# Kernel optimization log

Measured on AMD Instinct MI355X. Metric: run time of the kernel, lower is better.

## Reference

```python
import jax, jax.numpy as jnp
import numpy as np
from jax import lax

DN = ('NCHW', 'HWIO', 'NCHW')

def conv(x, w, b, stride, pad):
    y = lax.conv_general_dilated(x, w, (stride, stride), ((pad, pad), (pad, pad)),
                                 dimension_numbers=DN)
    return y + b[None, :, None, None]

def deconv(x, w, b):
    # PyTorch ConvTranspose2d(k=4, s=2, p=1) == conv with lhs_dilation=2, padding=k-1-p=2
    y = lax.conv_general_dilated(x, w, (1, 1), ((2, 2), (2, 2)), lhs_dilation=(2, 2),
                                 dimension_numbers=DN)
    return y + b[None, :, None, None]

def setup_inputs() -> dict:
    key = jax.random.key(0)
    ks = jax.random.split(key, 16)
    B, K, D = 4096, 512, 64
    def w(k, shape, fan_in):
        s = 1.0 / np.sqrt(fan_in)
        return jax.random.uniform(k, shape, jnp.float32, -s, s)
    return {
        'x': jax.random.uniform(ks[0], (B, 1, 28, 28), jnp.float32),
        # encoder
        'w1': w(ks[1], (4, 4, 1, 32), 4 * 4 * 1),  'b1': w(ks[2], (32,), 4 * 4 * 1),
        'w2': w(ks[3], (4, 4, 32, 64), 4 * 4 * 32), 'b2': w(ks[4], (64,), 4 * 4 * 32),
        'w3': w(ks[5], (1, 1, 64, D), 64),          'b3': w(ks[6], (D,), 64),
        # codebook, init uniform(-1/K, 1/K) as in the torch module
        'codebook': jax.random.uniform(ks[7], (K, D), jnp.float32, -1.0 / K, 1.0 / K),
        # decoder
        'dw0': w(ks[8], (1, 1, D, 64), D),          'db0': w(ks[9], (64,), D),
        'dw1': w(ks[10], (4, 4, 64, 32), 4 * 4 * 64), 'db1': w(ks[11], (32,), 4 * 4 * 64),
        'dw2': w(ks[12], (4, 4, 32, 1), 4 * 4 * 32),  'db2': w(ks[13], (1,), 4 * 4 * 32),
    }

def vector_quantize(z_perm, codebook, commitment_cost=0.25):
    # z_perm: [B, H, W, D]
    D = codebook.shape[1]
    flat_z = z_perm.reshape(-1, D)                                      # [N, D]
    dists = (jnp.sum(flat_z * flat_z, axis=1, keepdims=True)
             + jnp.sum(codebook * codebook, axis=1)
             - 2.0 * flat_z @ codebook.T)                               # [N, K]
    indices = jnp.argmin(dists, axis=1)                                 # [N]
    quantized = codebook[indices].reshape(z_perm.shape)                 # [B, H, W, D]
    e_latent = jnp.mean((quantized - lax.stop_gradient(z_perm)) ** 2)
    q_latent = jnp.mean((z_perm - lax.stop_gradient(quantized)) ** 2)
    vq_loss = e_latent + commitment_cost * q_latent
    quantized_st = z_perm + lax.stop_gradient(quantized - z_perm)
    return quantized_st, vq_loss, indices.reshape(z_perm.shape[:-1])

def reference(x, w1, b1, w2, b2, w3, b3, codebook, dw0, db0, dw1, db1, dw2, db2):
    # encoder: 28 -> 14 -> 7
    h = jax.nn.relu(conv(x, w1, b1, 2, 1))
    h = jax.nn.relu(conv(h, w2, b2, 2, 1))
    z = conv(h, w3, b3, 1, 0)                        # [B, D, 7, 7]
    z_perm = jnp.transpose(z, (0, 2, 3, 1))          # [B, 7, 7, D]
    zq_perm, vq_loss, indices = vector_quantize(z_perm, codebook)
    z_q = jnp.transpose(zq_perm, (0, 3, 1, 2))       # [B, D, 7, 7]
    # decoder: 7 -> 14 -> 28
    d = conv(z_q, dw0, db0, 1, 0)
    d = jax.nn.relu(deconv(d, dw1, db1))
    recon = jax.nn.sigmoid(deconv(d, dw2, db2))
    recon = recon[:, :, :28, :28]
    return recon, z, z_q, vq_loss, indices
```

## Files before the change

kernel.cpp:

```cpp
#include <hip/hip_runtime.h>


#define NB 4096

__device__ __forceinline__ float4 f4fma(float s, float4 w, float4 a) {
  a.x = fmaf(s, w.x, a.x); a.y = fmaf(s, w.y, a.y);
  a.z = fmaf(s, w.z, a.z); a.w = fmaf(s, w.w, a.w);
  return a;
}
__device__ __forceinline__ float4 f4relu(float4 a) {
  a.x = fmaxf(a.x, 0.f); a.y = fmaxf(a.y, 0.f);
  a.z = fmaxf(a.z, 0.f); a.w = fmaxf(a.w, 0.f);
  return a;
}
__device__ __forceinline__ float4 f4addrn(float4 a, float4 b) {
  a.x = __fadd_rn(a.x, b.x); a.y = __fadd_rn(a.y, b.y);
  a.z = __fadd_rn(a.z, b.z); a.w = __fadd_rn(a.w, b.w);
  return a;
}

__device__ __forceinline__ float np_sumsq64(const float* v) {
  float r[8];
#pragma unroll
  for (int j = 0; j < 8; ++j) r[j] = __fmul_rn(v[j], v[j]);
#pragma unroll
  for (int i = 8; i < 64; i += 8)
#pragma unroll
    for (int j = 0; j < 8; ++j) r[j] = __fadd_rn(r[j], __fmul_rn(v[i + j], v[i + j]));
  return __fadd_rn(__fadd_rn(__fadd_rn(r[0], r[1]), __fadd_rn(r[2], r[3])),
                   __fadd_rn(__fadd_rn(r[4], r[5]), __fadd_rn(r[6], r[7])));
}

__global__ __launch_bounds__(256) void k0_init(const float* __restrict__ cb,
                                               float* __restrict__ cn,
                                               float* __restrict__ loss) {
  int t = threadIdx.x;
  if (t == 0) *loss = 0.f;
  for (int k = t; k < 512; k += 256) cn[k] = np_sumsq64(&cb[k * 64]);
}

__global__ __launch_bounds__(256) void k1_conv1(const float* __restrict__ x,
                                                const float* __restrict__ w1,
                                                const float* __restrict__ b1,
                                                float* __restrict__ h1) {
  __shared__ float xs[784];
  __shared__ float wl[512];
  __shared__ float bs[32];
  int n = blockIdx.x, t = threadIdx.x;
  for (int j = t; j < 784; j += 256) xs[j] = x[n * 784 + j];
  for (int j = t; j < 512; j += 256) wl[j] = w1[j];
  if (t < 32) bs[t] = b1[t];
  __syncthreads();
  int c = t & 31, pg = t >> 5;
  for (int s = pg; s < 196; s += 8) {
    int oh = s / 14, ow = s % 14;
    float acc = 0.f;
#pragma unroll
    for (int kh = 0; kh < 4; ++kh) {
      int ih = 2 * oh - 1 + kh;
      if (ih < 0 || ih >= 28) continue;
#pragma unroll
      for (int kw = 0; kw < 4; ++kw) {
        int iw = 2 * ow - 1 + kw;
        if (iw < 0 || iw >= 28) continue;
        acc = fmaf(xs[ih * 28 + iw], wl[(kh * 4 + kw) * 32 + c], acc);
      }
    }
    acc = __fadd_rn(acc, bs[c]);
    h1[(n * 196 + s) * 32 + c] = fmaxf(acc, 0.f);
  }
}

__global__ __launch_bounds__(256) void k2_conv2(const float* __restrict__ h1,
                                                const float* __restrict__ w2,
                                                const float* __restrict__ b2,
                                                float* __restrict__ h2) {
  __shared__ float4 xs4[2 * 2049];
  int nb = blockIdx.x, t = threadIdx.x;
  size_t n0 = (size_t)nb * 2;
  for (int j = t; j < 4098; j += 256) xs4[j] = make_float4(0.f, 0.f, 0.f, 0.f);
  __syncthreads();
  for (int j = t; j < 1568; j += 256) {
    int p = j >> 3, c4 = j & 7;
    int ihp = p / 14 + 1, iwp = p % 14 + 1;
    int chunk = (c4 * 16 + ihp) * 16 + (iwp & 1) * 8 + (iwp >> 1);
    xs4[chunk] = *(const float4*)(h1 + n0 * 6272 + p * 32 + c4 * 4);
    xs4[2049 + chunk] = *(const float4*)(h1 + (n0 + 1) * 6272 + p * 32 + c4 * 4);
  }
  __syncthreads();
  int l = t & 63;
  int co0 = __builtin_amdgcn_readfirstlane((t >> 6) * 16);
  int img = l >> 5, pt = l & 31;
  int oh0 = pt >> 3, ow = pt & 7;
  int imgoff = img * 2049;
  bool v0 = (ow < 7);
  bool v1 = (ow < 7) && (oh0 + 4 < 7);
  float4 A0[4], A1[4];
#pragma unroll
  for (int g = 0; g < 4; ++g) { A0[g] = make_float4(0.f, 0.f, 0.f, 0.f); A1[g] = A0[g]; }
#pragma unroll 1
  for (int kk = 0; kk < 16; ++kk) {
    int kh = kk >> 2, kw = kk & 3;
    int cc = 2 * ow + kw; if (cc > 15) cc = 15;
    int off = (cc & 1) * 8 + (cc >> 1);
    int rc0 = 2 * oh0 + kh;
    int rc1 = rc0 + 8; if (rc1 > 15) rc1 = 15;
    int b0 = imgoff + rc0 * 16 + off;
    int b1 = imgoff + rc1 * 16 + off;
    int wb = __builtin_amdgcn_readfirstlane(kk * 2048 + co0);
#pragma unroll 2
    for (int c4 = 0; c4 < 8; ++c4) {
      float4 x0 = xs4[b0 + c4 * 256];
      float4 x1 = xs4[b1 + c4 * 256];
      float xa0[4] = {x0.x, x0.y, x0.z, x0.w};
      float xa1[4] = {x1.x, x1.y, x1.z, x1.w};
      const float* wk = w2 + wb + c4 * 256;
#pragma unroll
      for (int j = 0; j < 4; ++j) {
#pragma unroll
        for (int g = 0; g < 4; ++g) {
          float4 wv4;
          wv4.x = wk[j * 64 + g * 4 + 0]; wv4.y = wk[j * 64 + g * 4 + 1];
          wv4.z = wk[j * 64 + g * 4 + 2]; wv4.w = wk[j * 64 + g * 4 + 3];
          A0[g] = f4fma(xa0[j], wv4, A0[g]);
          A1[g] = f4fma(xa1[j], wv4, A1[g]);
        }
      }
    }
  }
  float4 bias[4];
#pragma unroll
  for (int g = 0; g < 4; ++g) bias[g] = *(const float4*)&b2[co0 + g * 4];
  if (v0) {
    size_t ob = ((n0 + img) * 49 + oh0 * 7 + ow) * 64 + co0;
#pragma unroll
    for (int g = 0; g < 4; ++g)
      *(float4*)&h2[ob + g * 4] = f4relu(f4addrn(A0[g], bias[g]));
  }
  if (v1) {
    size_t ob = ((n0 + img) * 49 + (oh0 + 4) * 7 + ow) * 64 + co0;
#pragma unroll
    for (int g = 0; g < 4; ++g)
      *(float4*)&h2[ob + g * 4] = f4relu(f4addrn(A1[g], bias[g]));
  }
}

__global__ __launch_bounds__(256) void k_pw(const float* __restrict__ xin,
                                            const float* __restrict__ w,
                                            const float* __restrict__ bias,
                                            float* __restrict__ yout) {
  __shared__ float tile[256 * 65];
  int t = threadIdx.x;
  long m0 = (long)blockIdx.x * 256;
  for (int j = t; j < 16384; j += 256) tile[(j >> 6) * 65 + (j & 63)] = xin[m0 * 64 + j];
  __syncthreads();
  float xr[64];
#pragma unroll
  for (int ci = 0; ci < 64; ++ci) xr[ci] = tile[t * 65 + ci];
  for (int g = 0; g < 4; ++g) {
    float4 z4 = make_float4(0.f, 0.f, 0.f, 0.f);
    float4 a0 = z4, a1 = z4, a2 = z4, a3 = z4;
#pragma unroll
    for (int ci = 0; ci < 64; ++ci) {
      float xv = xr[ci];
      const float* wr = &w[ci * 64 + g * 16];
      a0 = f4fma(xv, *(const float4*)&wr[0], a0);
      a1 = f4fma(xv, *(const float4*)&wr[4], a1);
      a2 = f4fma(xv, *(const float4*)&wr[8], a2);
      a3 = f4fma(xv, *(const float4*)&wr[12], a3);
    }
    a0 = f4addrn(a0, *(const float4*)&bias[g * 16 + 0]);
    a1 = f4addrn(a1, *(const float4*)&bias[g * 16 + 4]);
    a2 = f4addrn(a2, *(const float4*)&bias[g * 16 + 8]);
    a3 = f4addrn(a3, *(const float4*)&bias[g * 16 + 12]);
    float* dst = &tile[t * 65 + g * 16];
    dst[0] = a0.x; dst[1] = a0.y; dst[2] = a0.z; dst[3] = a0.w;
    dst[4] = a1.x; dst[5] = a1.y; dst[6] = a1.z; dst[7] = a1.w;
    dst[8] = a2.x; dst[9] = a2.y; dst[10] = a2.z; dst[11] = a2.w;
    dst[12] = a3.x; dst[13] = a3.y; dst[14] = a3.z; dst[15] = a3.w;
  }
  __syncthreads();
  for (int j = t; j < 16384; j += 256) yout[m0 * 64 + j] = tile[(j >> 6) * 65 + (j & 63)];
}

__global__ __launch_bounds__(256) void k4_vq(const float* __restrict__ zin,
                                             const float* __restrict__ cb,
                                             const float* __restrict__ cn,
                                             float* __restrict__ zq_nhwc,
                                             float* __restrict__ outz,
                                             float* __restrict__ outzq,
                                             float* __restrict__ outidx,
                                             float* __restrict__ loss) {
  __shared__ float tile[256 * 65];
  __shared__ float red[4];
  int t = threadIdx.x;
  long m0 = (long)blockIdx.x * 256;
  for (int j = t; j < 16384; j += 256) tile[(j >> 6) * 65 + (j & 63)] = zin[m0 * 64 + j];
  __syncthreads();
  float zr[64];
#pragma unroll
  for (int ci = 0; ci < 64; ++ci) zr[ci] = tile[t * 65 + ci];
  unsigned m = (unsigned)(m0 + t);
  unsigned n = m / 49u, sp = m % 49u;
  float* zob = outz + (size_t)n * 3136 + sp;
#pragma unroll
  for (int ci = 0; ci < 64; ++ci) zob[ci * 49] = zr[ci];
  float sz = np_sumsq64(zr);
  float minv = 3.4e38f; int mini = 0;
  for (int k = 0; k < 512; ++k) {
    float d = 0.f;
#pragma unroll
    for (int ci = 0; ci < 64; ci += 4) {
      float4 c4 = *(const float4*)&cb[k * 64 + ci];
      d = fmaf(zr[ci + 0], c4.x, d);
      d = fmaf(zr[ci + 1], c4.y, d);
      d = fmaf(zr[ci + 2], c4.z, d);
      d = fmaf(zr[ci + 3], c4.w, d);
    }
    float dist = __fsub_rn(__fadd_rn(sz, cn[k]), __fmul_rn(2.f, d));
    if (dist < minv) { minv = dist; mini = k; }
  }
  outidx[m] = (float)mini;
  float* qob = outzq + (size_t)n * 3136 + sp;
  float lsum = 0.f;
#pragma unroll
  for (int ci = 0; ci < 64; ci += 4) {
    float4 q4 = *(const float4*)&cb[mini * 64 + ci];
    float* dst = &tile[t * 65 + ci];
    dst[0] = q4.x; dst[1] = q4.y; dst[2] = q4.z; dst[3] = q4.w;
    qob[(ci + 0) * 49] = q4.x; qob[(ci + 1) * 49] = q4.y;
    qob[(ci + 2) * 49] = q4.z; qob[(ci + 3) * 49] = q4.w;
    float e0 = q4.x - zr[ci + 0], e1 = q4.y - zr[ci + 1];
    float e2 = q4.z - zr[ci + 2], e3 = q4.w - zr[ci + 3];
    lsum = fmaf(e0, e0, lsum); lsum = fmaf(e1, e1, lsum);
    lsum = fmaf(e2, e2, lsum); lsum = fmaf(e3, e3, lsum);
  }
#pragma unroll
  for (int off = 32; off > 0; off >>= 1) lsum += __shfl_down(lsum, off);
  int wid = t >> 6, lane = t & 63;
  if (lane == 0) red[wid] = lsum;
  __syncthreads();
  if (t == 0) atomicAdd(loss, red[0] + red[1] + red[2] + red[3]);
  for (int j = t; j < 16384; j += 256) zq_nhwc[m0 * 64 + j] = tile[(j >> 6) * 65 + (j & 63)];
}

__global__ __launch_bounds__(64) void k_lossfin(const float* __restrict__ loss,
                                                float* __restrict__ out) {
  if (threadIdx.x == 0) out[0] = loss[0] * (1.25f / 12845056.f);
}

__global__ __launch_bounds__(256) void k6_deconv1(const float* __restrict__ d0,
                                                  const float* __restrict__ dw1,
                                                  const float* __restrict__ db1,
                                                  float* __restrict__ d1) {
  __shared__ float4 xs4[2 * 1297];
  int nb = blockIdx.x, t = threadIdx.x;
  size_t n0 = (size_t)nb * 2;
  for (int j = t; j < 2594; j += 256) xs4[j] = make_float4(0.f, 0.f, 0.f, 0.f);
  __syncthreads();
  for (int j = t; j < 784; j += 256) {
    int p = j >> 4, c4 = j & 15;
    int chunk = c4 * 81 + (p / 7 + 1) * 9 + (p % 7 + 1);
    xs4[chunk] = *(const float4*)(d0 + n0 * 3136 + p * 64 + c4 * 4);
    xs4[1297 + chunk] = *(const float4*)(d0 + (n0 + 1) * 3136 + p * 64 + c4 * 4);
  }
  __syncthreads();
  int l = t & 63;
  int ph = __builtin_amdgcn_readfirstlane(t >> 6);
  int ra = ph >> 1, rb = ph & 1;
  int img = l >> 5, pt = l & 31;
  bool v1 = (pt + 32 < 49);
  int p1 = v1 ? pt + 32 : 48;
  int mh0 = pt / 7, mw0 = pt % 7;
  int mh1 = p1 / 7, mw1 = p1 % 7;
  int imgoff = img * 1297;
  float4 A0[8], A1[8];
#pragma unroll
  for (int g = 0; g < 8; ++g) { A0[g] = make_float4(0.f, 0.f, 0.f, 0.f); A1[g] = A0[g]; }
#pragma unroll 1
  for (int tap = 0; tap < 4; ++tap) {
    int th = tap >> 1, tw = tap & 1;
    int kh = 2 * th + ra, kw = 2 * tw + rb;
    int b0 = imgoff + (mh0 + th + ra) * 9 + (mw0 + tw + rb);
    int b1 = imgoff + (mh1 + th + ra) * 9 + (mw1 + tw + rb);
    int wb = __builtin_amdgcn_readfirstlane((kh * 4 + kw) * 2048);
#pragma unroll 1
    for (int c4 = 0; c4 < 16; ++c4) {
      float4 x0 = xs4[b0 + c4 * 81];
      float4 x1 = xs4[b1 + c4 * 81];
      float xa0[4] = {x0.x, x0.y, x0.z, x0.w};
      float xa1[4] = {x1.x, x1.y, x1.z, x1.w};
      const float* wk = dw1 + wb + c4 * 128;
#pragma unroll
      for (int j = 0; j < 4; ++j) {
#pragma unroll
        for (int g = 0; g < 8; ++g) {
          float4 wv4;
          wv4.x = wk[j * 32 + g * 4 + 0]; wv4.y = wk[j * 32 + g * 4 + 1];
          wv4.z = wk[j * 32 + g * 4 + 2]; wv4.w = wk[j * 32 + g * 4 + 3];
          A0[g] = f4fma(xa0[j], wv4, A0[g]);
          A1[g] = f4fma(xa1[j], wv4, A1[g]);
        }
      }
    }
  }
  int oh0 = 2 * mh0 + ra, ow0 = 2 * mw0 + rb;
  size_t ob0 = ((n0 + img) * 196 + (size_t)(oh0 * 14 + ow0)) * 32;
#pragma unroll
  for (int g = 0; g < 8; ++g) {
    float4 bg = *(const float4*)&db1[g * 4];
    *(float4*)&d1[ob0 + g * 4] = f4relu(f4addrn(A0[g], bg));
  }
  if (v1) {
    int oh1 = 2 * mh1 + ra, ow1 = 2 * mw1 + rb;
    size_t ob1 = ((n0 + img) * 196 + (size_t)(oh1 * 14 + ow1)) * 32;
#pragma unroll
    for (int g = 0; g < 8; ++g) {
      float4 bg = *(const float4*)&db1[g * 4];
      *(float4*)&d1[ob1 + g * 4] = f4relu(f4addrn(A1[g], bg));
    }
  }
}

__global__ __launch_bounds__(256) void k7_deconv2(const float* __restrict__ d1,
                                                  const float* __restrict__ dw2,
                                                  const float* __restrict__ db2,
                                                  float* __restrict__ recon) {
  __shared__ float xs[196 * 36];
  __shared__ float wl[512];
  int n = blockIdx.x, t = threadIdx.x;
  for (int j = t; j < 6272; j += 256) xs[(j >> 5) * 36 + (j & 31)] = d1[(size_t)n * 6272 + j];
  for (int j = t; j < 512; j += 256) wl[j] = dw2[j];
  __syncthreads();
  float bias = db2[0];
  for (int j = t; j < 392; j += 256) {
    int ra = j / 196, rem = j % 196;
    int mh = rem / 14, mw = rem % 14;
    float acc0 = bias, acc1 = bias;
    bool vm = (mw >= 1), vp = (mw + 1 < 14);
#pragma unroll
    for (int th = 0; th < 2; ++th) {
      int ih = mh + th - 1 + ra;
      if (ih < 0 || ih >= 14) continue;
      int kh = 2 * th + ra;
#pragma unroll
      for (int ci = 0; ci < 32; ci += 4) {
        float4 z4 = make_float4(0.f, 0.f, 0.f, 0.f);
        float4 xm = vm ? *(float4*)&xs[(ih * 14 + mw - 1) * 36 + ci] : z4;
        float4 x0 = *(float4*)&xs[(ih * 14 + mw) * 36 + ci];
        float4 xp = vp ? *(float4*)&xs[(ih * 14 + mw + 1) * 36 + ci] : z4;
        float4 wk0 = *(float4*)&wl[(kh * 4 + 0) * 32 + ci];
        float4 wk1 = *(float4*)&wl[(kh * 4 + 1) * 32 + ci];
        float4 wk2 = *(float4*)&wl[(kh * 4 + 2) * 32 + ci];
        float4 wk3 = *(float4*)&wl[(kh * 4 + 3) * 32 + ci];
        acc0 = fmaf(xm.x, wk0.x, acc0); acc0 = fmaf(xm.y, wk0.y, acc0);
        acc0 = fmaf(xm.z, wk0.z, acc0); acc0 = fmaf(xm.w, wk0.w, acc0);
        acc0 = fmaf(x0.x, wk2.x, acc0); acc0 = fmaf(x0.y, wk2.y, acc0);
        acc0 = fmaf(x0.z, wk2.z, acc0); acc0 = fmaf(x0.w, wk2.w, acc0);
        acc1 = fmaf(x0.x, wk1.x, acc1); acc1 = fmaf(x0.y, wk1.y, acc1);
        acc1 = fmaf(x0.z, wk1.z, acc1); acc1 = fmaf(x0.w, wk1.w, acc1);
        acc1 = fmaf(xp.x, wk3.x, acc1); acc1 = fmaf(xp.y, wk3.y, acc1);
        acc1 = fmaf(xp.z, wk3.z, acc1); acc1 = fmaf(xp.w, wk3.w, acc1);
      }
    }
    float r0 = 1.f / (1.f + __expf(-acc0));
    float r1 = 1.f / (1.f + __expf(-acc1));
    int oh = 2 * mh + ra;
    *(float2*)&recon[(size_t)n * 784 + oh * 28 + 2 * mw] = make_float2(r0, r1);
  }
}

extern "C" void kernel_launch(void* const* d_in, const int* in_sizes, int n_in,
                              void* d_out, int out_size, void* d_ws, size_t ws_size,
                              hipStream_t stream) {
  const float* x   = (const float*)d_in[0];
  const float* w1  = (const float*)d_in[1];
  const float* b1  = (const float*)d_in[2];
  const float* w2  = (const float*)d_in[3];
  const float* b2  = (const float*)d_in[4];
  const float* w3  = (const float*)d_in[5];
  const float* b3  = (const float*)d_in[6];
  const float* cb  = (const float*)d_in[7];
  const float* dw0 = (const float*)d_in[8];
  const float* db0 = (const float*)d_in[9];
  const float* dw1 = (const float*)d_in[10];
  const float* db1 = (const float*)d_in[11];
  const float* dw2 = (const float*)d_in[12];
  const float* db2 = (const float*)d_in[13];
  float* out = (float*)d_out;
  float* ws  = (float*)d_ws;

  float* h1   = ws;
  float* h2   = ws + 25690112;
  float* zb   = ws + 38535168;
  float* cn   = ws + 51380224;
  float* loss = ws + 51380736;

  float* recon   = out;
  float* zout    = out + 3211264;
  float* zqout   = out + 16056320;
  float* lossout = out + 28901376;
  float* idxout  = out + 28901377;

  k0_init<<<1, 256, 0, stream>>>(cb, cn, loss);
  k1_conv1<<<NB, 256, 0, stream>>>(x, w1, b1, h1);
  k2_conv2<<<NB / 2, 256, 0, stream>>>(h1, w2, b2, h2);
  k_pw<<<784, 256, 0, stream>>>(h2, w3, b3, zb);
  k4_vq<<<784, 256, 0, stream>>>(zb, cb, cn, h2, zout, zqout, idxout, loss);
  k_lossfin<<<1, 64, 0, stream>>>(loss, lossout);
  k_pw<<<784, 256, 0, stream>>>(h2, dw0, db0, zb);
  k6_deconv1<<<NB / 2, 256, 0, stream>>>(zb, dw1, db1, h1);
  k7_deconv2<<<NB, 256, 0, stream>>>(h1, dw2, db2, recon);
}
```

Baseline: 1.255 ms.

## Fuse decoder 1x1 conv into VQ kernel and drop shared-memory transposes

Folds the decoder pointwise conv (dw0/db0) into the VQ kernel, so each thread applies it directly to its selected codebook row and writes the result in place into the z buffer. This removes one kernel launch and a full round trip of the quantized NHWC tensor. The pointwise and VQ kernels now read and write 64-float rows per thread with float4 accesses instead of staging through padded shared tiles. The VQ distance loop now handles four codewords per iteration, and the loss reduction uses a per-wave atomic with no block-level sync. In exchange, per-thread accesses are strided by 256 bytes rather than coalesced, and register pressure rises from the 64 accumulators.

```diff
diff --git a/kernel.cpp b/kernel.cpp
--- a/kernel.cpp
+++ b/kernel.cpp
@@ -149,99 +149,117 @@
                                             const float* __restrict__ w,
                                             const float* __restrict__ bias,
                                             float* __restrict__ yout) {
-  __shared__ float tile[256 * 65];
-  int t = threadIdx.x;
-  long m0 = (long)blockIdx.x * 256;
-  for (int j = t; j < 16384; j += 256) tile[(j >> 6) * 65 + (j & 63)] = xin[m0 * 64 + j];
-  __syncthreads();
+  size_t m = (size_t)blockIdx.x * 256 + threadIdx.x;
+  const float* xp = xin + m * 64;
   float xr[64];
 #pragma unroll
-  for (int ci = 0; ci < 64; ++ci) xr[ci] = tile[t * 65 + ci];
-  for (int g = 0; g < 4; ++g) {
-    float4 z4 = make_float4(0.f, 0.f, 0.f, 0.f);
-    float4 a0 = z4, a1 = z4, a2 = z4, a3 = z4;
-#pragma unroll
-    for (int ci = 0; ci < 64; ++ci) {
-      float xv = xr[ci];
-      const float* wr = &w[ci * 64 + g * 16];
-      a0 = f4fma(xv, *(const float4*)&wr[0], a0);
-      a1 = f4fma(xv, *(const float4*)&wr[4], a1);
-      a2 = f4fma(xv, *(const float4*)&wr[8], a2);
-      a3 = f4fma(xv, *(const float4*)&wr[12], a3);
-    }
-    a0 = f4addrn(a0, *(const float4*)&bias[g * 16 + 0]);
-    a1 = f4addrn(a1, *(const float4*)&bias[g * 16 + 4]);
-    a2 = f4addrn(a2, *(const float4*)&bias[g * 16 + 8]);
-    a3 = f4addrn(a3, *(const float4*)&bias[g * 16 + 12]);
-    float* dst = &tile[t * 65 + g * 16];
-    dst[0] = a0.x; dst[1] = a0.y; dst[2] = a0.z; dst[3] = a0.w;
-    dst[4] = a1.x; dst[5] = a1.y; dst[6] = a1.z; dst[7] = a1.w;
-    dst[8] = a2.x; dst[9] = a2.y; dst[10] = a2.z; dst[11] = a2.w;
-    dst[12] = a3.x; dst[13] = a3.y; dst[14] = a3.z; dst[15] = a3.w;
-  }
-  __syncthreads();
-  for (int j = t; j < 16384; j += 256) yout[m0 * 64 + j] = tile[(j >> 6) * 65 + (j & 63)];
-}
-
-__global__ __launch_bounds__(256) void k4_vq(const float* __restrict__ zin,
+  for (int c4 = 0; c4 < 16; ++c4) {
+    float4 v = *(const float4*)(xp + c4 * 4);
+    xr[c4 * 4 + 0] = v.x; xr[c4 * 4 + 1] = v.y;
+    xr[c4 * 4 + 2] = v.z; xr[c4 * 4 + 3] = v.w;
+  }
+  float4 A[16];
+#pragma unroll
+  for (int g = 0; g < 16; ++g) A[g] = make_float4(0.f, 0.f, 0.f, 0.f);
+#pragma unroll 1
+  for (int ci = 0; ci < 64; ++ci) {
+    float xv = xr[ci];
+    const float* wr = w + ci * 64;
+#pragma unroll
+    for (int g = 0; g < 16; ++g)
+      A[g] = f4fma(xv, *(const float4*)(wr + g * 4), A[g]);
+  }
+  float* yp = yout + m * 64;
+#pragma unroll
+  for (int g = 0; g < 16; ++g)
+    *(float4*)(yp + g * 4) = f4addrn(A[g], *(const float4*)(bias + g * 4));
+}
+
+__global__ __launch_bounds__(256) void k4_vq(float* __restrict__ zbuf,
                                              const float* __restrict__ cb,
                                              const float* __restrict__ cn,
-                                             float* __restrict__ zq_nhwc,
+                                             const float* __restrict__ dw0,
+                                             const float* __restrict__ db0,
                                              float* __restrict__ outz,
                                              float* __restrict__ outzq,
                                              float* __restrict__ outidx,
                                              float* __restrict__ loss) {
-  __shared__ float tile[256 * 65];
-  __shared__ float red[4];
   int t = threadIdx.x;
-  long m0 = (long)blockIdx.x * 256;
-  for (int j = t; j < 16384; j += 256) tile[(j >> 6) * 65 + (j & 63)] = zin[m0 * 64 + j];
-  __syncthreads();
+  size_t m = (size_t)blockIdx.x * 256 + t;
+  const float* zp = zbuf + m * 64;
   float zr[64];
 #pragma unroll
-  for (int ci = 0; ci < 64; ++ci) zr[ci] = tile[t * 65 + ci];
-  unsigned m = (unsigned)(m0 + t);
-  unsigned n = m / 49u, sp = m % 49u;
+  for (int c4 = 0; c4 < 16; ++c4) {
+    float4 v = *(const float4*)(zp + c4 * 4);
+    zr[c4 * 4 + 0] = v.x; zr[c4 * 4 + 1] = v.y;
+    zr[c4 * 4 + 2] = v.z; zr[c4 * 4 + 3] = v.w;
+  }
+  unsigned n = (unsigned)(m / 49u), sp = (unsigned)(m % 49u);
   float* zob = outz + (size_t)n * 3136 + sp;
 #pragma unroll
   for (int ci = 0; ci < 64; ++ci) zob[ci * 49] = zr[ci];
   float sz = np_sumsq64(zr);
   float minv = 3.4e38f; int mini = 0;
-  for (int k = 0; k < 512; ++k) {
-    float d = 0.f;
+#pragma unroll 1
+  for (int k = 0; k < 512; k += 4) {
+    const float* cp = cb + (size_t)k * 64;
+    float d0_ = 0.f, d1_ = 0.f, d2_ = 0.f, d3_ = 0.f;
 #pragma unroll
     for (int ci = 0; ci < 64; ci += 4) {
-      float4 c4 = *(const float4*)&cb[k * 64 + ci];
-      d = fmaf(zr[ci + 0], c4.x, d);
-      d = fmaf(zr[ci + 1], c4.y, d);
-      d = fmaf(zr[ci + 2], c4.z, d);
-      d = fmaf(zr[ci + 3], c4.w, d);
-    }
-    float dist = __fsub_rn(__fadd_rn(sz, cn[k]), __fmul_rn(2.f, d));
-    if (dist < minv) { minv = dist; mini = k; }
+      float4 a = *(const float4*)(cp + ci);
+      float4 b = *(const float4*)(cp + 64 + ci);
+      float4 c = *(const float4*)(cp + 128 + ci);
+      float4 e = *(const float4*)(cp + 192 + ci);
+      d0_ = fmaf(zr[ci], a.x, d0_); d0_ = fmaf(zr[ci + 1], a.y, d0_);
+      d0_ = fmaf(zr[ci + 2], a.z, d0_); d0_ = fmaf(zr[ci + 3], a.w, d0_);
+      d1_ = fmaf(zr[ci], b.x, d1_); d1_ = fmaf(zr[ci + 1], b.y, d1_);
+      d1_ = fmaf(zr[ci + 2], b.z, d1_); d1_ = fmaf(zr[ci + 3], b.w, d1_);
+      d2_ = fmaf(zr[ci], c.x, d2_); d2_ = fmaf(zr[ci + 1], c.y, d2_);
+      d2_ = fmaf(zr[ci + 2], c.z, d2_); d2_ = fmaf(zr[ci + 3], c.w, d2_);
+      d3_ = fmaf(zr[ci], e.x, d3_); d3_ = fmaf(zr[ci + 1], e.y, d3_);
+      d3_ = fmaf(zr[ci + 2], e.z, d3_); d3_ = fmaf(zr[ci + 3], e.w, d3_);
+    }
+    float q0 = __fsub_rn(__fadd_rn(sz, cn[k + 0]), __fmul_rn(2.f, d0_));
+    float q1 = __fsub_rn(__fadd_rn(sz, cn[k + 1]), __fmul_rn(2.f, d1_));
+    float q2 = __fsub_rn(__fadd_rn(sz, cn[k + 2]), __fmul_rn(2.f, d2_));
+    float q3 = __fsub_rn(__fadd_rn(sz, cn[k + 3]), __fmul_rn(2.f, d3_));
+    if (q0 < minv) { minv = q0; mini = k; }
+    if (q1 < minv) { minv = q1; mini = k + 1; }
+    if (q2 < minv) { minv = q2; mini = k + 2; }
+    if (q3 < minv) { minv = q3; mini = k + 3; }
   }
   outidx[m] = (float)mini;
   float* qob = outzq + (size_t)n * 3136 + sp;
+  const float* qrow = cb + (size_t)mini * 64;
   float lsum = 0.f;
-#pragma unroll
-  for (int ci = 0; ci < 64; ci += 4) {
-    float4 q4 = *(const float4*)&cb[mini * 64 + ci];
-    float* dst = &tile[t * 65 + ci];
-    dst[0] = q4.x; dst[1] = q4.y; dst[2] = q4.z; dst[3] = q4.w;
-    qob[(ci + 0) * 49] = q4.x; qob[(ci + 1) * 49] = q4.y;
-    qob[(ci + 2) * 49] = q4.z; qob[(ci + 3) * 49] = q4.w;
-    float e0 = q4.x - zr[ci + 0], e1 = q4.y - zr[ci + 1];
-    float e2 = q4.z - zr[ci + 2], e3 = q4.w - zr[ci + 3];
+  float4 A[16];
+#pragma unroll
+  for (int g = 0; g < 16; ++g) A[g] = make_float4(0.f, 0.f, 0.f, 0.f);
+#pragma unroll
+  for (int c4 = 0; c4 < 16; ++c4) {
+    float4 q4 = *(const float4*)(qrow + c4 * 4);
+    qob[(c4 * 4 + 0) * 49] = q4.x; qob[(c4 * 4 + 1) * 49] = q4.y;
+    qob[(c4 * 4 + 2) * 49] = q4.z; qob[(c4 * 4 + 3) * 49] = q4.w;
+    float e0 = q4.x - zr[c4 * 4 + 0], e1 = q4.y - zr[c4 * 4 + 1];
+    float e2 = q4.z - zr[c4 * 4 + 2], e3 = q4.w - zr[c4 * 4 + 3];
     lsum = fmaf(e0, e0, lsum); lsum = fmaf(e1, e1, lsum);
     lsum = fmaf(e2, e2, lsum); lsum = fmaf(e3, e3, lsum);
+    float qa[4] = {q4.x, q4.y, q4.z, q4.w};
+#pragma unroll
+    for (int j = 0; j < 4; ++j) {
+      const float* wr = dw0 + (c4 * 4 + j) * 64;
+#pragma unroll
+      for (int g = 0; g < 16; ++g)
+        A[g] = f4fma(qa[j], *(const float4*)(wr + g * 4), A[g]);
+    }
   }
 #pragma unroll
   for (int off = 32; off > 0; off >>= 1) lsum += __shfl_down(lsum, off);
-  int wid = t >> 6, lane = t & 63;
-  if (lane == 0) red[wid] = lsum;
-  __syncthreads();
-  if (t == 0) atomicAdd(loss, red[0] + red[1] + red[2] + red[3]);
-  for (int j = t; j < 16384; j += 256) zq_nhwc[m0 * 64 + j] = tile[(j >> 6) * 65 + (j & 63)];
+  if ((t & 63) == 0) atomicAdd(loss, lsum);
+  float* dst = zbuf + m * 64;
+#pragma unroll
+  for (int g = 0; g < 16; ++g)
+    *(float4*)(dst + g * 4) = f4addrn(A[g], *(const float4*)(db0 + g * 4));
 }
 
 __global__ __launch_bounds__(64) void k_lossfin(const float* __restrict__ loss,
@@ -406,9 +424,9 @@
   k1_conv1<<<NB, 256, 0, stream>>>(x, w1, b1, h1);
   k2_conv2<<<NB / 2, 256, 0, stream>>>(h1, w2, b2, h2);
   k_pw<<<784, 256, 0, stream>>>(h2, w3, b3, zb);
-  k4_vq<<<784, 256, 0, stream>>>(zb, cb, cn, h2, zout, zqout, idxout, loss);
+  k4_vq<<<784, 256, 0, stream>>>(zb, cb, cn, dw0, db0,
+                                 zout, zqout, idxout, loss);
   k_lossfin<<<1, 64, 0, stream>>>(loss, lossout);
-  k_pw<<<784, 256, 0, stream>>>(h2, dw0, db0, zb);
   k6_deconv1<<<NB / 2, 256, 0, stream>>>(zb, dw1, db1, h1);
   k7_deconv2<<<NB, 256, 0, stream>>>(h1, dw2, db2, recon);
 }
```

Result: slower. 2.316 ms (+84.6%).

## Stage codebook chunks in LDS and process two rows per thread in VQ

Applied to the files above, without the earlier changes.

The VQ kernel now handles 512 rows per block, with two latent vectors per thread, and loads the codebook into shared memory in 64-entry chunks instead of reading it from global memory in the inner loop. Each codebook float4 is then reused across two rows and two codes per iteration. The grid halves to 392 blocks and staging goes through a smaller LDS tile in four passes. This raises register pressure (128 floats of z per thread) and lowers block count, so occupancy and parallelism across the GPU drop.

```diff
diff --git a/kernel.cpp b/kernel.cpp
--- a/kernel.cpp
+++ b/kernel.cpp
@@ -191,57 +191,129 @@
                                              float* __restrict__ outzq,
                                              float* __restrict__ outidx,
                                              float* __restrict__ loss) {
-  __shared__ float tile[256 * 65];
+  __shared__ float lds[8320];
   __shared__ float red[4];
   int t = threadIdx.x;
-  long m0 = (long)blockIdx.x * 256;
-  for (int j = t; j < 16384; j += 256) tile[(j >> 6) * 65 + (j & 63)] = zin[m0 * 64 + j];
-  __syncthreads();
-  float zr[64];
-#pragma unroll
-  for (int ci = 0; ci < 64; ++ci) zr[ci] = tile[t * 65 + ci];
-  unsigned m = (unsigned)(m0 + t);
-  unsigned n = m / 49u, sp = m % 49u;
-  float* zob = outz + (size_t)n * 3136 + sp;
-#pragma unroll
-  for (int ci = 0; ci < 64; ++ci) zob[ci * 49] = zr[ci];
-  float sz = np_sumsq64(zr);
-  float minv = 3.4e38f; int mini = 0;
-  for (int k = 0; k < 512; ++k) {
-    float d = 0.f;
-#pragma unroll
-    for (int ci = 0; ci < 64; ci += 4) {
-      float4 c4 = *(const float4*)&cb[k * 64 + ci];
-      d = fmaf(zr[ci + 0], c4.x, d);
-      d = fmaf(zr[ci + 1], c4.y, d);
-      d = fmaf(zr[ci + 2], c4.z, d);
-      d = fmaf(zr[ci + 3], c4.w, d);
-    }
-    float dist = __fsub_rn(__fadd_rn(sz, cn[k]), __fmul_rn(2.f, d));
-    if (dist < minv) { minv = dist; mini = k; }
-  }
-  outidx[m] = (float)mini;
-  float* qob = outzq + (size_t)n * 3136 + sp;
+  size_t m0 = (size_t)blockIdx.x * 512;
+  float zrA[64], zrB[64];
+
+#define K4_STAGE_IN(S, ZR)                                                    \
+  {                                                                           \
+    __syncthreads();                                                          \
+    const float* src = zin + (m0 + (S) * 128) * 64;                           \
+    for (int j4 = t; j4 < 2048; j4 += 256) {                                  \
+      int row = j4 >> 4, col = (j4 & 15) * 4;                                 \
+      *(float4*)&lds[row * 65 + col] = *(const float4*)(src + j4 * 4);        \
+    }                                                                         \
+    __syncthreads();                                                          \
+    if ((t >> 7) == ((S) & 1)) {                                              \
+      int r = t & 127;                                                        \
+      _Pragma("unroll")                                                       \
+      for (int ci = 0; ci < 64; ci += 4) {                                    \
+        float4 v = *(float4*)&lds[r * 65 + ci];                               \
+        ZR[ci] = v.x; ZR[ci + 1] = v.y; ZR[ci + 2] = v.z; ZR[ci + 3] = v.w;   \
+      }                                                                       \
+    }                                                                         \
+  }
+
+  K4_STAGE_IN(0, zrA)
+  K4_STAGE_IN(1, zrA)
+  K4_STAGE_IN(2, zrB)
+  K4_STAGE_IN(3, zrB)
+
+  float szA = np_sumsq64(zrA), szB = np_sumsq64(zrB);
+  float minA = 3.4e38f, minB = 3.4e38f;
+  int miA = 0, miB = 0;
+#pragma unroll 1
+  for (int ch = 0; ch < 8; ++ch) {
+    __syncthreads();
+    for (int j = t; j < 4096; j += 256) lds[j] = cb[ch * 4096 + j];
+    if (ch == 0)
+      for (int j = t; j < 512; j += 256) lds[4096 + j] = cn[j];
+    __syncthreads();
+#pragma unroll 1
+    for (int k = 0; k < 64; k += 2) {
+      const float* r0 = &lds[k * 64];
+      const float* r1 = r0 + 64;
+      float dA0 = 0.f, dA1 = 0.f, dB0 = 0.f, dB1 = 0.f;
+#pragma unroll
+      for (int ci = 0; ci < 64; ci += 4) {
+        float4 c0 = *(const float4*)(r0 + ci);
+        float4 c1 = *(const float4*)(r1 + ci);
+        dA0 = fmaf(zrA[ci], c0.x, dA0); dA0 = fmaf(zrA[ci + 1], c0.y, dA0);
+        dA0 = fmaf(zrA[ci + 2], c0.z, dA0); dA0 = fmaf(zrA[ci + 3], c0.w, dA0);
+        dB0 = fmaf(zrB[ci], c0.x, dB0); dB0 = fmaf(zrB[ci + 1], c0.y, dB0);
+        dB0 = fmaf(zrB[ci + 2], c0.z, dB0); dB0 = fmaf(zrB[ci + 3], c0.w, dB0);
+        dA1 = fmaf(zrA[ci], c1.x, dA1); dA1 = fmaf(zrA[ci + 1], c1.y, dA1);
+        dA1 = fmaf(zrA[ci + 2], c1.z, dA1); dA1 = fmaf(zrA[ci + 3], c1.w, dA1);
+        dB1 = fmaf(zrB[ci], c1.x, dB1); dB1 = fmaf(zrB[ci + 1], c1.y, dB1);
+        dB1 = fmaf(zrB[ci + 2], c1.z, dB1); dB1 = fmaf(zrB[ci + 3], c1.w, dB1);
+      }
+      float cn0 = lds[4096 + ch * 64 + k];
+      float cn1 = lds[4096 + ch * 64 + k + 1];
+      float qA0 = __fsub_rn(__fadd_rn(szA, cn0), __fmul_rn(2.f, dA0));
+      float qA1 = __fsub_rn(__fadd_rn(szA, cn1), __fmul_rn(2.f, dA1));
+      float qB0 = __fsub_rn(__fadd_rn(szB, cn0), __fmul_rn(2.f, dB0));
+      float qB1 = __fsub_rn(__fadd_rn(szB, cn1), __fmul_rn(2.f, dB1));
+      int kk = ch * 64 + k;
+      if (qA0 < minA) { minA = qA0; miA = kk; }
+      if (qA1 < minA) { minA = qA1; miA = kk + 1; }
+      if (qB0 < minB) { minB = qB0; miB = kk; }
+      if (qB1 < minB) { minB = qB1; miB = kk + 1; }
+    }
+  }
+  outidx[m0 + t] = (float)miA;
+  outidx[m0 + 256 + t] = (float)miB;
+  {
+    unsigned mA = (unsigned)(m0 + t), mB = (unsigned)(m0 + 256 + t);
+    unsigned nA = mA / 49u, spA = mA % 49u;
+    unsigned nB = mB / 49u, spB = mB % 49u;
+    float* zoA = outz + (size_t)nA * 3136 + spA;
+    float* zoB = outz + (size_t)nB * 3136 + spB;
+#pragma unroll
+    for (int ci = 0; ci < 64; ++ci) { zoA[ci * 49] = zrA[ci]; zoB[ci * 49] = zrB[ci]; }
+  }
   float lsum = 0.f;
-#pragma unroll
-  for (int ci = 0; ci < 64; ci += 4) {
-    float4 q4 = *(const float4*)&cb[mini * 64 + ci];
-    float* dst = &tile[t * 65 + ci];
-    dst[0] = q4.x; dst[1] = q4.y; dst[2] = q4.z; dst[3] = q4.w;
-    qob[(ci + 0) * 49] = q4.x; qob[(ci + 1) * 49] = q4.y;
-    qob[(ci + 2) * 49] = q4.z; qob[(ci + 3) * 49] = q4.w;
-    float e0 = q4.x - zr[ci + 0], e1 = q4.y - zr[ci + 1];
-    float e2 = q4.z - zr[ci + 2], e3 = q4.w - zr[ci + 3];
-    lsum = fmaf(e0, e0, lsum); lsum = fmaf(e1, e1, lsum);
-    lsum = fmaf(e2, e2, lsum); lsum = fmaf(e3, e3, lsum);
-  }
+#define K4_STAGE_OUT(S, ZR, MI)                                               \
+  {                                                                           \
+    __syncthreads();                                                          \
+    if ((t >> 7) == ((S) & 1)) {                                              \
+      int r = t & 127;                                                        \
+      unsigned mm = (unsigned)(m0 + (S) * 128 + r);                           \
+      unsigned nn = mm / 49u, ss = mm % 49u;                                  \
+      float* qo = outzq + (size_t)nn * 3136 + ss;                             \
+      const float* qr = cb + (size_t)(MI) * 64;                               \
+      _Pragma("unroll")                                                       \
+      for (int ci = 0; ci < 64; ci += 4) {                                    \
+        float4 q4 = *(const float4*)(qr + ci);                                \
+        *(float4*)&lds[r * 65 + ci] = q4;                                     \
+        qo[(ci + 0) * 49] = q4.x; qo[(ci + 1) * 49] = q4.y;                   \
+        qo[(ci + 2) * 49] = q4.z; qo[(ci + 3) * 49] = q4.w;                   \
+        float e0 = q4.x - ZR[ci], e1 = q4.y - ZR[ci + 1];                     \
+        float e2 = q4.z - ZR[ci + 2], e3 = q4.w - ZR[ci + 3];                 \
+        lsum = fmaf(e0, e0, lsum); lsum = fmaf(e1, e1, lsum);                 \
+        lsum = fmaf(e2, e2, lsum); lsum = fmaf(e3, e3, lsum);                 \
+      }                                                                       \
+    }                                                                         \
+    __syncthreads();                                                          \
+    float* dstg = zq_nhwc + (m0 + (S) * 128) * 64;                            \
+    for (int j4 = t; j4 < 2048; j4 += 256) {                                  \
+      int row = j4 >> 4, col = (j4 & 15) * 4;                                 \
+      *(float4*)(dstg + j4 * 4) = *(float4*)&lds[row * 65 + col];             \
+    }                                                                         \
+  }
+  K4_STAGE_OUT(0, zrA, miA)
+  K4_STAGE_OUT(1, zrA, miA)
+  K4_STAGE_OUT(2, zrB, miB)
+  K4_STAGE_OUT(3, zrB, miB)
 #pragma unroll
   for (int off = 32; off > 0; off >>= 1) lsum += __shfl_down(lsum, off);
   int wid = t >> 6, lane = t & 63;
   if (lane == 0) red[wid] = lsum;
   __syncthreads();
   if (t == 0) atomicAdd(loss, red[0] + red[1] + red[2] + red[3]);
-  for (int j = t; j < 16384; j += 256) zq_nhwc[m0 * 64 + j] = tile[(j >> 6) * 65 + (j & 63)];
+#undef K4_STAGE_IN
+#undef K4_STAGE_OUT
 }
 
 __global__ __launch_bounds__(64) void k_lossfin(const float* __restrict__ loss,
@@ -406,7 +478,7 @@
   k1_conv1<<<NB, 256, 0, stream>>>(x, w1, b1, h1);
   k2_conv2<<<NB / 2, 256, 0, stream>>>(h1, w2, b2, h2);
   k_pw<<<784, 256, 0, stream>>>(h2, w3, b3, zb);
-  k4_vq<<<784, 256, 0, stream>>>(zb, cb, cn, h2, zout, zqout, idxout, loss);
+  k4_vq<<<392, 256, 0, stream>>>(zb, cb, cn, h2, zout, zqout, idxout, loss);
   k_lossfin<<<1, 64, 0, stream>>>(loss, lossout);
   k_pw<<<784, 256, 0, stream>>>(h2, dw0, db0, zb);
   k6_deconv1<<<NB / 2, 256, 0, stream>>>(zb, dw1, db1, h1);
```

Measured after the change: 1.208 ms. 1.04x faster.
